# Optimization experiments

Measured on AMD Instinct MI355X. Metric: run time of the kernel, lower is better.

## Reference

```python
import jax, jax.numpy as jnp
import numpy as np

D_MODEL = 1024
N_HEADS = 16
D_HEAD = D_MODEL // N_HEADS


def setup_inputs() -> dict:
    key = jax.random.key(0)
    ks = jax.random.split(key, 5)
    B, T = 2, 2048
    x = jax.random.normal(ks[0], (B, T, D_MODEL), dtype=jnp.float32)
    s = 1.0 / np.sqrt(D_MODEL)
    W_qkv = jax.random.normal(ks[1], (D_MODEL, 3 * D_MODEL), dtype=jnp.float32) * s
    b_qkv = jnp.zeros((3 * D_MODEL,), dtype=jnp.float32)
    W_proj = jax.random.normal(ks[2], (D_MODEL, D_MODEL), dtype=jnp.float32) * s
    b_proj = jnp.zeros((D_MODEL,), dtype=jnp.float32)
    return {"x": x, "W_qkv": W_qkv, "b_qkv": b_qkv, "W_proj": W_proj, "b_proj": b_proj}


def reference(x, W_qkv, b_qkv, W_proj, b_proj):
    B, T, C = x.shape
    qkv = x @ W_qkv + b_qkv                      # [B,T,3C]
    q, k, v = jnp.split(qkv, 3, axis=-1)
    # [B,T,C] -> [B,H,T,Dh]
    def to_heads(t):
        return t.reshape(B, T, N_HEADS, D_HEAD).transpose(0, 2, 1, 3)
    q, k, v = to_heads(q), to_heads(k), to_heads(v)
    scale = 1.0 / np.sqrt(D_HEAD).astype(np.float32)
    scores = jnp.einsum('bhqd,bhkd->bhqk', q, k) * scale  # [B,H,T,T]
    causal = jnp.tril(jnp.ones((T, T), dtype=bool))
    scores = jnp.where(causal, scores, -jnp.inf)
    attn = jax.nn.softmax(scores, axis=-1)
    out = jnp.einsum('bhqk,bhkd->bhqd', attn, v)          # [B,H,T,Dh]
    out = out.transpose(0, 2, 1, 3).reshape(B, T, C)
    return out @ W_proj + b_proj
```

## Files before the change

kernel.cpp:

```cpp
#include <hip/hip_runtime.h>
#include <hip/hip_bf16.h>
#include <cstdint>


using u16 = unsigned short;
using u32 = unsigned int;

typedef __bf16 bf16x8 __attribute__((ext_vector_type(8)));
typedef float f32x4 __attribute__((ext_vector_type(4)));

#define AS1 __attribute__((address_space(1)))
#define AS3 __attribute__((address_space(3)))

__device__ __forceinline__ u16 f2bf(float f) {
  u32 u = __float_as_uint(f);
  u += 0x7fffu + ((u >> 16) & 1u);
  return (u16)(u >> 16);
}
__device__ __forceinline__ u32 cvtpk(float a, float b) {
  u32 r;
  asm("v_cvt_pk_bf16_f32 %0, %1, %2" : "=v"(r) : "v"(a), "v"(b));
  return r;
}

__global__ __launch_bounds__(256) void prep(const float* __restrict__ x,
                                            u16* __restrict__ xb,
                                            const float* __restrict__ W0,
                                            u16* __restrict__ T0,
                                            const float* __restrict__ W1,
                                            u16* __restrict__ T1) {
  const int bx = blockIdx.x;
  const int tid = threadIdx.x;
  if (bx < 4096) {
    const int i = bx * 256 + tid;
    float4 v = ((const float4*)x)[i];
    ushort4 o;
    o.x = f2bf(v.x); o.y = f2bf(v.y); o.z = f2bf(v.z); o.w = f2bf(v.w);
    ((ushort4*)xb)[i] = o;
    return;
  }
  __shared__ float t[32][33];
  const int idx = bx - 4096;
  const int bxx = idx & 127, by = idx >> 7;
  const float* W; u16* Wt; int N, n0;
  if (bxx < 96) { W = W0; Wt = T0; N = 3072; n0 = bxx * 32; }
  else          { W = W1; Wt = T1; N = 1024; n0 = (bxx - 96) * 32; }
  const int k0 = by * 32;
  const int tx = tid & 31, ty = tid >> 5;
#pragma unroll
  for (int i = 0; i < 4; ++i)
    t[ty + i * 8][tx] = W[(size_t)(k0 + ty + i * 8) * N + n0 + tx];
  __syncthreads();
#pragma unroll
  for (int i = 0; i < 4; ++i)
    Wt[(size_t)(n0 + ty + i * 8) * 1024 + k0 + tx] = f2bf(t[tx][ty + i * 8]);
}

#define MFMA16 __builtin_amdgcn_mfma_f32_16x16x32_bf16

__global__ __launch_bounds__(256, 2) void gemm_qkv(const u16* __restrict__ A,
                                                   const u16* __restrict__ Bt,
                                                   const float* __restrict__ bias,
                                                   u16* __restrict__ qb,
                                                   u16* __restrict__ KF,
                                                   u16* __restrict__ VF,
                                                   float sc_val) {
  constexpr int NT = 16;
  constexpr int BUFO = 5 * 4096;
  __shared__ __align__(16) u16 sm[2 * BUFO];

  const int tid  = threadIdx.x;
  const int lane = tid & 63;
  const int w    = tid >> 6;
  const int quad = lane >> 4;
  const int l15  = lane & 15;

  const int bid = blockIdx.x;
  const int xcd = bid & 7, c = bid >> 3;
  const int mt = xcd * 4 + (c & 3);
  const int nt = c >> 2;
  const int bm = mt * 128, bn = nt * 192;

  const int wc = w * 48;

  const int srow = tid >> 3;
  const int scol = (((tid & 7) ^ ((tid >> 3) & 7)) << 3);

#define STAGEA(ch, ktile, bufo)                                                 \
  do {                                                                          \
    const u16* _s = A + (size_t)(bm + (ch) * 64 + srow) * 1024 +                \
                    ((ktile) << 6) + scol;                                      \
    u16* _d = sm + (bufo) + (ch) * 4096 + tid * 8;                              \
    __builtin_amdgcn_global_load_lds((AS1 const void*)_s, (AS3 void*)_d,        \
                                     16, 0, 0);                                 \
    __builtin_amdgcn_global_load_lds((AS1 const void*)(_s + (32 << 10)),        \
                                     (AS3 void*)(_d + 2048), 16, 0, 0);         \
  } while (0)
#define STAGEB(ch, ktile, bufo)                                                 \
  do {                                                                          \
    const u16* _s = Bt + (size_t)(bn + (ch) * 64 + srow) * 1024 +               \
                    ((ktile) << 6) + scol;                                      \
    u16* _d = sm + (bufo) + (2 + (ch)) * 4096 + tid * 8;                        \
    __builtin_amdgcn_global_load_lds((AS1 const void*)_s, (AS3 void*)_d,        \
                                     16, 0, 0);                                 \
    __builtin_amdgcn_global_load_lds((AS1 const void*)(_s + (32 << 10)),        \
                                     (AS3 void*)(_d + 2048), 16, 0, 0);         \
  } while (0)

  int abase_lo[4], abase_hi[4], bbase[3];
#pragma unroll
  for (int mi = 0; mi < 4; ++mi) {
    abase_lo[mi] = 0 * 4096 + (mi * 16 + l15) * 64;
    abase_hi[mi] = 1 * 4096 + (mi * 16 + l15) * 64;
  }
#pragma unroll
  for (int ni = 0; ni < 3; ++ni) {
    const int rb = wc + ni * 16 + l15;
    bbase[ni] = (2 + (rb >> 6)) * 4096 + (rb & 63) * 64;
  }
  const int sw0 = ((quad ^ (l15 & 7)) << 3);
  const int sw1 = sw0 ^ 32;

  STAGEA(0, 0, 0); STAGEA(1, 0, 0);
  STAGEB(0, 0, 0); STAGEB(1, 0, 0); STAGEB(2, 0, 0);
  STAGEA(0, 1, BUFO); STAGEA(1, 1, BUFO);
  asm volatile("s_waitcnt vmcnt(4)" ::: "memory");
  __builtin_amdgcn_s_barrier();

  f32x4 acc[8][3] = {};
  bf16x8 alo[4][2], ahi[4][2], b[3][2];

#pragma unroll 2
  for (int j = 0; j < NT; ++j) {
    const int bo  = (j & 1) * BUFO;
    const int nbo = bo ^ BUFO;
    const u16* smb = sm + bo;

#pragma unroll
    for (int mi = 0; mi < 4; ++mi) {
      alo[mi][0] = *(const bf16x8*)(smb + abase_lo[mi] + sw0);
      alo[mi][1] = *(const bf16x8*)(smb + abase_lo[mi] + sw1);
    }
#pragma unroll
    for (int ni = 0; ni < 2; ++ni) {
      b[ni][0] = *(const bf16x8*)(smb + bbase[ni] + sw0);
      b[ni][1] = *(const bf16x8*)(smb + bbase[ni] + sw1);
    }
#pragma unroll
    for (int mi = 0; mi < 4; ++mi) {
      ahi[mi][0] = *(const bf16x8*)(smb + abase_hi[mi] + sw0);
      ahi[mi][1] = *(const bf16x8*)(smb + abase_hi[mi] + sw1);
    }
    b[2][0] = *(const bf16x8*)(smb + bbase[2] + sw0);
    b[2][1] = *(const bf16x8*)(smb + bbase[2] + sw1);
    if (j + 1 < NT) { STAGEB(0, j + 1, nbo); STAGEB(1, j + 1, nbo); STAGEB(2, j + 1, nbo); }

    asm volatile("s_waitcnt lgkmcnt(10)" ::: "memory");
    __builtin_amdgcn_sched_barrier(0);
    __builtin_amdgcn_s_setprio(1);
#pragma unroll
    for (int mi = 0; mi < 4; ++mi)
#pragma unroll
      for (int ni = 0; ni < 2; ++ni) {
        acc[mi][ni] = MFMA16(alo[mi][0], b[ni][0], acc[mi][ni], 0, 0, 0);
        acc[mi][ni] = MFMA16(alo[mi][1], b[ni][1], acc[mi][ni], 0, 0, 0);
      }
    __builtin_amdgcn_s_setprio(0);
    asm volatile("s_waitcnt lgkmcnt(0)" ::: "memory");
    __builtin_amdgcn_sched_barrier(0);
    __builtin_amdgcn_s_barrier();
    if (j + 2 < NT) { STAGEA(0, j + 2, bo); STAGEA(1, j + 2, bo); }
    __builtin_amdgcn_s_setprio(1);
#pragma unroll
    for (int mi = 0; mi < 4; ++mi) {
      acc[mi][2] = MFMA16(alo[mi][0], b[2][0], acc[mi][2], 0, 0, 0);
      acc[mi][2] = MFMA16(alo[mi][1], b[2][1], acc[mi][2], 0, 0, 0);
      acc[4 + mi][0] = MFMA16(ahi[mi][0], b[0][0], acc[4 + mi][0], 0, 0, 0);
      acc[4 + mi][0] = MFMA16(ahi[mi][1], b[0][1], acc[4 + mi][0], 0, 0, 0);
    }
#pragma unroll
    for (int mi = 0; mi < 4; ++mi)
#pragma unroll
      for (int ni = 1; ni < 3; ++ni) {
        acc[4 + mi][ni] = MFMA16(ahi[mi][0], b[ni][0], acc[4 + mi][ni], 0, 0, 0);
        acc[4 + mi][ni] = MFMA16(ahi[mi][1], b[ni][1], acc[4 + mi][ni], 0, 0, 0);
      }
    __builtin_amdgcn_s_setprio(0);
    if (j + 2 < NT)
      asm volatile("s_waitcnt vmcnt(4)" ::: "memory");
    else
      asm volatile("s_waitcnt vmcnt(0)" ::: "memory");
    __builtin_amdgcn_s_barrier();
  }
#undef STAGEA
#undef STAGEB

  const int crow0 = bm + (quad << 2);
  const int ccol0 = bn + wc + l15;
#pragma unroll
  for (int ni = 0; ni < 3; ++ni) {
    const int n = ccol0 + ni * 16;
    const float bv = bias[n];
    if (n < 1024) {
#pragma unroll
      for (int mi = 0; mi < 8; ++mi) {
        const int m0 = crow0 + mi * 16;
#pragma unroll
        for (int r = 0; r < 4; ++r)
          qb[(size_t)(m0 + r) * 1024 + n] = f2bf((acc[mi][ni][r] + bv) * sc_val);
      }
    } else if (n < 2048) {
      const int hk = (n - 1024) >> 6;
      const int d  = (n - 1024) & 63;
      const int hh = d >> 5, qd = (d >> 3) & 3, jj = d & 7;
#pragma unroll
      for (int mi = 0; mi < 8; ++mi) {
#pragma unroll
        for (int r = 0; r < 4; ++r) {
          const int t  = crow0 + mi * 16 + r;
          const int bb = t >> 11, tt = t & 2047;
          const int kt = tt >> 6, mm = (tt >> 4) & 3, l = tt & 15;
          KF[((size_t)((bb * 16 + hk) * 32 + kt) * 8 + mm * 2 + hh) * 512 +
             (qd * 16 + l) * 8 + jj] = f2bf(acc[mi][ni][r] + bv);
        }
      }
    } else {
      const int hv = (n - 2048) >> 6;
      const int d  = (n - 2048) & 63;
      const int di = d >> 4, l = d & 15;
#pragma unroll
      for (int mi = 0; mi < 8; ++mi) {
        const int t  = crow0 + mi * 16;
        const int bb = t >> 11, tt = t & 2047;
        const int kt = tt >> 6, to = tt & 63;
        const int mq = to >> 4, qd2 = (to >> 2) & 3;
        const int hh = mq >> 1, jj = (mq & 1) * 4;
        uint2 o;
        o.x = cvtpk(acc[mi][ni][0] + bv, acc[mi][ni][1] + bv);
        o.y = cvtpk(acc[mi][ni][2] + bv, acc[mi][ni][3] + bv);
        *(uint2*)&VF[((size_t)((bb * 16 + hv) * 32 + kt) * 8 + hh * 4 + di) * 512 +
                     (qd2 * 16 + l) * 8 + jj] = o;
      }
    }
  }
}

__global__ __launch_bounds__(256, 2) void gemm_proj(const u16* __restrict__ A,
                                                    const u16* __restrict__ Bt,
                                                    const float* __restrict__ bias,
                                                    float* __restrict__ C) {
  constexpr int NT = 16;
  constexpr int BUFO = 3 * 4096;
  __shared__ __align__(16) u16 sm[2 * BUFO];

  const int tid  = threadIdx.x;
  const int lane = tid & 63;
  const int w    = tid >> 6;
  const int quad = lane >> 4;
  const int l15  = lane & 15;

  const int bid = blockIdx.x;
  const int xcd = bid & 7, c = bid >> 3;
  const int mt = xcd * 4 + (c & 3);
  const int nt = c >> 2;
  const int bm = mt * 128, bn = nt * 64;

  const int wr = (w >> 1) * 64;
  const int wcC = (w & 1) * 32;

  const int srow = tid >> 3;
  const int scol = (((tid & 7) ^ ((tid >> 3) & 7)) << 3);

#define PSTAGEA(ch, ktile, bufo)                                                \
  do {                                                                          \
    const u16* _s = A + (size_t)(bm + (ch) * 64 + srow) * 1024 +                \
                    ((ktile) << 6) + scol;                                      \
    u16* _d = sm + (bufo) + (ch) * 4096 + tid * 8;                              \
    __builtin_amdgcn_global_load_lds((AS1 const void*)_s, (AS3 void*)_d,        \
                                     16, 0, 0);                                 \
    __builtin_amdgcn_global_load_lds((AS1 const void*)(_s + (32 << 10)),        \
                                     (AS3 void*)(_d + 2048), 16, 0, 0);         \
  } while (0)
#define PSTAGEB(ktile, bufo)                                                    \
  do {                                                                          \
    const u16* _s = Bt + (size_t)(bn + srow) * 1024 + ((ktile) << 6) + scol;    \
    u16* _d = sm + (bufo) + 2 * 4096 + tid * 8;                                 \
    __builtin_amdgcn_global_load_lds((AS1 const void*)_s, (AS3 void*)_d,        \
                                     16, 0, 0);                                 \
    __builtin_amdgcn_global_load_lds((AS1 const void*)(_s + (32 << 10)),        \
                                     (AS3 void*)(_d + 2048), 16, 0, 0);         \
  } while (0)

  int abase[4], bbase[2];
#pragma unroll
  for (int mi = 0; mi < 4; ++mi)
    abase[mi] = (w >> 1) * 4096 + (mi * 16 + l15) * 64;
#pragma unroll
  for (int ni = 0; ni < 2; ++ni)
    bbase[ni] = 2 * 4096 + (wcC + ni * 16 + l15) * 64;
  const int sw0 = ((quad ^ (l15 & 7)) << 3);
  const int sw1 = sw0 ^ 32;

  PSTAGEA(0, 0, 0); PSTAGEA(1, 0, 0); PSTAGEB(0, 0);
  PSTAGEA(0, 1, BUFO); PSTAGEA(1, 1, BUFO);
  asm volatile("s_waitcnt vmcnt(4)" ::: "memory");
  __builtin_amdgcn_s_barrier();

  f32x4 acc[4][2] = {};
  bf16x8 a[4][2], b[2][2];

#pragma unroll 2
  for (int j = 0; j < NT; ++j) {
    const int bo  = (j & 1) * BUFO;
    const int nbo = bo ^ BUFO;
    const u16* smb = sm + bo;

#pragma unroll
    for (int mi = 0; mi < 4; ++mi) {
      a[mi][0] = *(const bf16x8*)(smb + abase[mi] + sw0);
      a[mi][1] = *(const bf16x8*)(smb + abase[mi] + sw1);
    }
#pragma unroll
    for (int ni = 0; ni < 2; ++ni) {
      b[ni][0] = *(const bf16x8*)(smb + bbase[ni] + sw0);
      b[ni][1] = *(const bf16x8*)(smb + bbase[ni] + sw1);
    }
    if (j + 1 < NT) PSTAGEB(j + 1, nbo);

    asm volatile("s_waitcnt lgkmcnt(2)" ::: "memory");
    __builtin_amdgcn_sched_barrier(0);
    __builtin_amdgcn_s_setprio(1);
#pragma unroll
    for (int mi = 0; mi < 4; ++mi) {
      acc[mi][0] = MFMA16(a[mi][0], b[0][0], acc[mi][0], 0, 0, 0);
      acc[mi][0] = MFMA16(a[mi][1], b[0][1], acc[mi][0], 0, 0, 0);
    }
    __builtin_amdgcn_s_setprio(0);
    asm volatile("s_waitcnt lgkmcnt(0)" ::: "memory");
    __builtin_amdgcn_sched_barrier(0);
    __builtin_amdgcn_s_barrier();
    if (j + 2 < NT) { PSTAGEA(0, j + 2, bo); PSTAGEA(1, j + 2, bo); }
    __builtin_amdgcn_s_setprio(1);
#pragma unroll
    for (int mi = 0; mi < 4; ++mi) {
      acc[mi][1] = MFMA16(a[mi][0], b[1][0], acc[mi][1], 0, 0, 0);
      acc[mi][1] = MFMA16(a[mi][1], b[1][1], acc[mi][1], 0, 0, 0);
    }
    __builtin_amdgcn_s_setprio(0);
    if (j + 2 < NT)
      asm volatile("s_waitcnt vmcnt(4)" ::: "memory");
    else
      asm volatile("s_waitcnt vmcnt(0)" ::: "memory");
    __builtin_amdgcn_s_barrier();
  }
#undef PSTAGEA
#undef PSTAGEB

  const int crow0 = bm + wr + (quad << 2);
  const int ccol0 = bn + wcC + l15;
#pragma unroll
  for (int ni = 0; ni < 2; ++ni) {
    const int n = ccol0 + ni * 16;
    const float bv = bias[n];
#pragma unroll
    for (int mi = 0; mi < 4; ++mi) {
      const int m0 = crow0 + mi * 16;
#pragma unroll
      for (int r = 0; r < 4; ++r)
        C[(size_t)(m0 + r) * 1024 + n] = acc[mi][ni][r] + bv;
    }
  }
}

__global__ __launch_bounds__(128, 2) void attn_bal(const u16* __restrict__ qb,
                                                   const u16* __restrict__ KF,
                                                   const u16* __restrict__ VF,
                                                   u16* __restrict__ out) {
  const int bid = blockIdx.x;
  const int c   = bid >> 3;
  const int u   = c & 31;
  const int bh  = (bid & 7) | ((c >> 5) << 3);
  const int b = bh >> 4, h = bh & 15;
  const int tid = threadIdx.x;
  const int lane = tid & 63;
  const int par  = tid >> 6;
  const int quad = lane >> 4;
  const int l15  = lane & 15;

  __shared__ float CB[64][41];

  const u16* qbase = qb + (size_t)b * 2048 * 1024 + h * 64;
  const size_t fb = (size_t)bh * 32 * 4096 + lane * 8;
  const u16* kfb = KF + fb;
  const u16* vfb = VF + fb;

  union { u32 u4[4]; bf16x8 v; } onesu;
  onesu.u4[0] = onesu.u4[1] = onesu.u4[2] = onesu.u4[3] = 0x3f803f80u;
  const bf16x8 onesf = onesu.v;

  u16* const outb = out + (size_t)b * 2048 * 1024 + h * 64 + l15;

  auto run_group = [&](int g32) {
    const int q0 = g32 * 32;
    const int ktmax = g32 >> 1;

    bf16x8 qf[2][2];
#pragma unroll
    for (int g = 0; g < 2; ++g)
#pragma unroll
      for (int hh = 0; hh < 2; ++hh)
        qf[g][hh] = *(const bf16x8*)(qbase + (size_t)(q0 + g * 16 + l15) * 1024 +
                                     hh * 32 + quad * 8);

    f32x4 accO[2][4] = {};
    f32x4 accL[2] = {};

    bf16x8 kA[4][2], kB[4][2], vA[2][4], vB[2][4];
    {
      const u16* kp = kfb + (size_t)par * 4096;
      const u16* vp = vfb + (size_t)par * 4096;
#pragma unroll
      for (int m = 0; m < 4; ++m)
#pragma unroll
        for (int hh = 0; hh < 2; ++hh)
          kA[m][hh] = *(const bf16x8*)(kp + (m * 2 + hh) * 512);
#pragma unroll
      for (int hh = 0; hh < 2; ++hh)
#pragma unroll
        for (int di = 0; di < 4; ++di)
          vA[hh][di] = *(const bf16x8*)(vp + (hh * 4 + di) * 512);
    }

    auto tile = [&](int kt, bf16x8 (&KC)[4][2], bf16x8 (&KN)[4][2],
                    bf16x8 (&VC)[2][4], bf16x8 (&VN)[2][4]) {
      const int ktn = (kt + 2 <= ktmax) ? kt + 2 : ktmax;
      const u16* kpn = kfb + (size_t)ktn * 4096;
      const u16* vpn = vfb + (size_t)ktn * 4096;
#pragma unroll
      for (int m = 0; m < 4; ++m)
#pragma unroll
        for (int hh = 0; hh < 2; ++hh)
          KN[m][hh] = *(const bf16x8*)(kpn + (m * 2 + hh) * 512);
#pragma unroll
      for (int hh = 0; hh < 2; ++hh)
#pragma unroll
        for (int di = 0; di < 4; ++di)
          VN[hh][di] = *(const bf16x8*)(vpn + (hh * 4 + di) * 512);

      const bool diag = (kt == ktmax);
      bf16x8 ap[2][2];
#pragma unroll
      for (int g = 0; g < 2; ++g) {
        f32x4 sT[4] = {};
#pragma unroll
        for (int m = 0; m < 4; ++m) {
          sT[m] = MFMA16(KC[m][0], qf[g][0], sT[m], 0, 0, 0);
          sT[m] = MFMA16(KC[m][1], qf[g][1], sT[m], 0, 0, 0);
        }
        float pv[4][4];
        if (diag) {
          const int qgl = q0 + g * 16 + l15;
#pragma unroll
          for (int m = 0; m < 4; ++m)
#pragma unroll
            for (int r = 0; r < 4; ++r) {
              const bool msk = (kt * 64 + m * 16 + quad * 4 + r) > qgl;
              pv[m][r] = msk ? 0.f : __builtin_amdgcn_exp2f(sT[m][r]);
            }
        } else {
#pragma unroll
          for (int m = 0; m < 4; ++m)
#pragma unroll
            for (int r = 0; r < 4; ++r)
              pv[m][r] = __builtin_amdgcn_exp2f(sT[m][r]);
        }
        union { u32 u4[4]; bf16x8 v; } t0, t1;
        t0.u4[0] = cvtpk(pv[0][0], pv[0][1]);
        t0.u4[1] = cvtpk(pv[0][2], pv[0][3]);
        t0.u4[2] = cvtpk(pv[1][0], pv[1][1]);
        t0.u4[3] = cvtpk(pv[1][2], pv[1][3]);
        t1.u4[0] = cvtpk(pv[2][0], pv[2][1]);
        t1.u4[1] = cvtpk(pv[2][2], pv[2][3]);
        t1.u4[2] = cvtpk(pv[3][0], pv[3][1]);
        t1.u4[3] = cvtpk(pv[3][2], pv[3][3]);
        ap[g][0] = t0.v;
        ap[g][1] = t1.v;
      }

#pragma unroll
      for (int hh = 0; hh < 2; ++hh)
#pragma unroll
        for (int di = 0; di < 4; ++di) {
          bf16x8 bv = VC[hh][di];
#pragma unroll
          for (int g = 0; g < 2; ++g)
            accO[g][di] = MFMA16(ap[g][hh], bv, accO[g][di], 0, 0, 0);
        }
#pragma unroll
      for (int g = 0; g < 2; ++g) {
        accL[g] = MFMA16(ap[g][0], onesf, accL[g], 0, 0, 0);
        accL[g] = MFMA16(ap[g][1], onesf, accL[g], 0, 0, 0);
      }
    };

    for (int kt = par; kt <= ktmax; ) {
      tile(kt, kA, kB, vA, vB); kt += 2;
      if (kt > ktmax) break;
      tile(kt, kB, kA, vB, vA); kt += 2;
    }

    if (par) {
      float* cb = CB[lane];
#pragma unroll
      for (int g = 0; g < 2; ++g) {
#pragma unroll
        for (int di = 0; di < 4; ++di)
#pragma unroll
          for (int r = 0; r < 4; ++r)
            cb[g * 16 + di * 4 + r] = accO[g][di][r];
#pragma unroll
        for (int r = 0; r < 4; ++r)
          cb[32 + g * 4 + r] = accL[g][r];
      }
    }
    __syncthreads();
    if (!par) {
      const float* cb = CB[lane];
#pragma unroll
      for (int g = 0; g < 2; ++g) {
#pragma unroll
        for (int di = 0; di < 4; ++di)
#pragma unroll
          for (int r = 0; r < 4; ++r)
            accO[g][di][r] += cb[g * 16 + di * 4 + r];
#pragma unroll
        for (int r = 0; r < 4; ++r)
          accL[g][r] += cb[32 + g * 4 + r];
      }
#pragma unroll
      for (int g = 0; g < 2; ++g)
#pragma unroll
        for (int r = 0; r < 4; ++r) {
          const float inv = 1.f / accL[g][r];
          const int q = q0 + g * 16 + quad * 4 + r;
          u16* op = outb + (size_t)q * 1024;
#pragma unroll
          for (int di = 0; di < 4; ++di)
            op[di * 16] = f2bf(accO[g][di][r] * inv);
        }
    }
    __syncthreads();
  };

  run_group(63 - u);
  run_group(u);
}

extern "C" void kernel_launch(void* const* d_in, const int* in_sizes, int n_in,
                              void* d_out, int out_size, void* d_ws, size_t ws_size,
                              hipStream_t stream) {
  const float* x     = (const float*)d_in[0];
  const float* Wqkv  = (const float*)d_in[1];
  const float* bqkv  = (const float*)d_in[2];
  const float* Wproj = (const float*)d_in[3];
  const float* bproj = (const float*)d_in[4];
  float* out = (float*)d_out;

  char* ws = (char*)d_ws;
  u16* xb     = (u16*)(ws);
  u16* wqkvT  = (u16*)(ws + 8388608);
  u16* wprojT = (u16*)(ws + 14680064);
  u16* qb     = (u16*)(ws + 16777216);
  u16* KF     = (u16*)(ws + 25165824);
  u16* VF     = (u16*)(ws + 33554432);
  u16* att    = (u16*)(ws + 41943040);

  constexpr float cs = 0.18033688011f;

  prep<<<8192, 256, 0, stream>>>(x, xb, Wqkv, wqkvT, Wproj, wprojT);

  gemm_qkv<<<dim3(512), 256, 0, stream>>>(xb, wqkvT, bqkv, qb, KF, VF, cs);

  attn_bal<<<dim3(1024), 128, 0, stream>>>(qb, KF, VF, att);

  gemm_proj<<<dim3(512), 256, 0, stream>>>(att, wprojT, bproj, out);
}
```

Measured before the change: 152.3 us.

## Split QKV GEMM tile across eight waves instead of four

Moves the QKV projection GEMM from 256 to 512 threads per block. Each wave now computes a 64x48 sub-tile instead of 128x48, and each thread issues one async global-to-LDS load per chunk instead of two. Accumulator and fragment register use per wave is halved to allow more waves per CU and better latency hiding. In exchange, each wave does less MFMA work per LDS read and barrier, and more threads take part in each block-wide sync.

```diff
diff --git a/kernel.cpp b/kernel.cpp
--- a/kernel.cpp
+++ b/kernel.cpp
@@ -58,7 +58,7 @@
 
 #define MFMA16 __builtin_amdgcn_mfma_f32_16x16x32_bf16
 
-__global__ __launch_bounds__(256, 2) void gemm_qkv(const u16* __restrict__ A,
+__global__ __launch_bounds__(512, 4) void gemm_qkv(const u16* __restrict__ A,
                                                    const u16* __restrict__ Bt,
                                                    const float* __restrict__ bias,
                                                    u16* __restrict__ qb,
@@ -81,41 +81,30 @@
   const int nt = c >> 2;
   const int bm = mt * 128, bn = nt * 192;
 
-  const int wc = w * 48;
+  const int wr  = (w >> 2) * 64;
+  const int wc2 = (w & 3) * 48;
 
   const int srow = tid >> 3;
   const int scol = (((tid & 7) ^ ((tid >> 3) & 7)) << 3);
 
 #define STAGEA(ch, ktile, bufo)                                                 \
-  do {                                                                          \
-    const u16* _s = A + (size_t)(bm + (ch) * 64 + srow) * 1024 +                \
-                    ((ktile) << 6) + scol;                                      \
-    u16* _d = sm + (bufo) + (ch) * 4096 + tid * 8;                              \
-    __builtin_amdgcn_global_load_lds((AS1 const void*)_s, (AS3 void*)_d,        \
-                                     16, 0, 0);                                 \
-    __builtin_amdgcn_global_load_lds((AS1 const void*)(_s + (32 << 10)),        \
-                                     (AS3 void*)(_d + 2048), 16, 0, 0);         \
-  } while (0)
+  __builtin_amdgcn_global_load_lds(                                             \
+      (AS1 const void*)(A + (size_t)(bm + (ch) * 64 + srow) * 1024 +            \
+                        ((ktile) << 6) + scol),                                 \
+      (AS3 void*)(sm + (bufo) + (ch) * 4096 + tid * 8), 16, 0, 0)
 #define STAGEB(ch, ktile, bufo)                                                 \
-  do {                                                                          \
-    const u16* _s = Bt + (size_t)(bn + (ch) * 64 + srow) * 1024 +               \
-                    ((ktile) << 6) + scol;                                      \
-    u16* _d = sm + (bufo) + (2 + (ch)) * 4096 + tid * 8;                        \
-    __builtin_amdgcn_global_load_lds((AS1 const void*)_s, (AS3 void*)_d,        \
-                                     16, 0, 0);                                 \
-    __builtin_amdgcn_global_load_lds((AS1 const void*)(_s + (32 << 10)),        \
-                                     (AS3 void*)(_d + 2048), 16, 0, 0);         \
-  } while (0)
-
-  int abase_lo[4], abase_hi[4], bbase[3];
-#pragma unroll
-  for (int mi = 0; mi < 4; ++mi) {
-    abase_lo[mi] = 0 * 4096 + (mi * 16 + l15) * 64;
-    abase_hi[mi] = 1 * 4096 + (mi * 16 + l15) * 64;
-  }
+  __builtin_amdgcn_global_load_lds(                                             \
+      (AS1 const void*)(Bt + (size_t)(bn + (ch) * 64 + srow) * 1024 +           \
+                        ((ktile) << 6) + scol),                                 \
+      (AS3 void*)(sm + (bufo) + (2 + (ch)) * 4096 + tid * 8), 16, 0, 0)
+
+  int abase[4], bbase[3];
+#pragma unroll
+  for (int mi = 0; mi < 4; ++mi)
+    abase[mi] = (w >> 2) * 4096 + (mi * 16 + l15) * 64;
 #pragma unroll
   for (int ni = 0; ni < 3; ++ni) {
-    const int rb = wc + ni * 16 + l15;
+    const int rb = wc2 + ni * 16 + l15;
     bbase[ni] = (2 + (rb >> 6)) * 4096 + (rb & 63) * 64;
   }
   const int sw0 = ((quad ^ (l15 & 7)) << 3);
@@ -124,11 +113,11 @@
   STAGEA(0, 0, 0); STAGEA(1, 0, 0);
   STAGEB(0, 0, 0); STAGEB(1, 0, 0); STAGEB(2, 0, 0);
   STAGEA(0, 1, BUFO); STAGEA(1, 1, BUFO);
-  asm volatile("s_waitcnt vmcnt(4)" ::: "memory");
+  asm volatile("s_waitcnt vmcnt(2)" ::: "memory");
   __builtin_amdgcn_s_barrier();
 
-  f32x4 acc[8][3] = {};
-  bf16x8 alo[4][2], ahi[4][2], b[3][2];
+  f32x4 acc[4][3] = {};
+  bf16x8 a[4][2], b[3][2];
 
 #pragma unroll 2
   for (int j = 0; j < NT; ++j) {
@@ -138,33 +127,24 @@
 
 #pragma unroll
     for (int mi = 0; mi < 4; ++mi) {
-      alo[mi][0] = *(const bf16x8*)(smb + abase_lo[mi] + sw0);
-      alo[mi][1] = *(const bf16x8*)(smb + abase_lo[mi] + sw1);
-    }
-#pragma unroll
-    for (int ni = 0; ni < 2; ++ni) {
+      a[mi][0] = *(const bf16x8*)(smb + abase[mi] + sw0);
+      a[mi][1] = *(const bf16x8*)(smb + abase[mi] + sw1);
+    }
+#pragma unroll
+    for (int ni = 0; ni < 3; ++ni) {
       b[ni][0] = *(const bf16x8*)(smb + bbase[ni] + sw0);
       b[ni][1] = *(const bf16x8*)(smb + bbase[ni] + sw1);
     }
-#pragma unroll
-    for (int mi = 0; mi < 4; ++mi) {
-      ahi[mi][0] = *(const bf16x8*)(smb + abase_hi[mi] + sw0);
-      ahi[mi][1] = *(const bf16x8*)(smb + abase_hi[mi] + sw1);
-    }
-    b[2][0] = *(const bf16x8*)(smb + bbase[2] + sw0);
-    b[2][1] = *(const bf16x8*)(smb + bbase[2] + sw1);
     if (j + 1 < NT) { STAGEB(0, j + 1, nbo); STAGEB(1, j + 1, nbo); STAGEB(2, j + 1, nbo); }
 
-    asm volatile("s_waitcnt lgkmcnt(10)" ::: "memory");
+    asm volatile("s_waitcnt lgkmcnt(4)" ::: "memory");
     __builtin_amdgcn_sched_barrier(0);
     __builtin_amdgcn_s_setprio(1);
 #pragma unroll
-    for (int mi = 0; mi < 4; ++mi)
-#pragma unroll
-      for (int ni = 0; ni < 2; ++ni) {
-        acc[mi][ni] = MFMA16(alo[mi][0], b[ni][0], acc[mi][ni], 0, 0, 0);
-        acc[mi][ni] = MFMA16(alo[mi][1], b[ni][1], acc[mi][ni], 0, 0, 0);
-      }
+    for (int mi = 0; mi < 4; ++mi) {
+      acc[mi][0] = MFMA16(a[mi][0], b[0][0], acc[mi][0], 0, 0, 0);
+      acc[mi][0] = MFMA16(a[mi][1], b[0][1], acc[mi][0], 0, 0, 0);
+    }
     __builtin_amdgcn_s_setprio(0);
     asm volatile("s_waitcnt lgkmcnt(0)" ::: "memory");
     __builtin_amdgcn_sched_barrier(0);
@@ -173,21 +153,14 @@
     __builtin_amdgcn_s_setprio(1);
 #pragma unroll
     for (int mi = 0; mi < 4; ++mi) {
-      acc[mi][2] = MFMA16(alo[mi][0], b[2][0], acc[mi][2], 0, 0, 0);
-      acc[mi][2] = MFMA16(alo[mi][1], b[2][1], acc[mi][2], 0, 0, 0);
-      acc[4 + mi][0] = MFMA16(ahi[mi][0], b[0][0], acc[4 + mi][0], 0, 0, 0);
-      acc[4 + mi][0] = MFMA16(ahi[mi][1], b[0][1], acc[4 + mi][0], 0, 0, 0);
-    }
-#pragma unroll
-    for (int mi = 0; mi < 4; ++mi)
-#pragma unroll
-      for (int ni = 1; ni < 3; ++ni) {
-        acc[4 + mi][ni] = MFMA16(ahi[mi][0], b[ni][0], acc[4 + mi][ni], 0, 0, 0);
-        acc[4 + mi][ni] = MFMA16(ahi[mi][1], b[ni][1], acc[4 + mi][ni], 0, 0, 0);
-      }
+      acc[mi][1] = MFMA16(a[mi][0], b[1][0], acc[mi][1], 0, 0, 0);
+      acc[mi][1] = MFMA16(a[mi][1], b[1][1], acc[mi][1], 0, 0, 0);
+      acc[mi][2] = MFMA16(a[mi][0], b[2][0], acc[mi][2], 0, 0, 0);
+      acc[mi][2] = MFMA16(a[mi][1], b[2][1], acc[mi][2], 0, 0, 0);
+    }
     __builtin_amdgcn_s_setprio(0);
     if (j + 2 < NT)
-      asm volatile("s_waitcnt vmcnt(4)" ::: "memory");
+      asm volatile("s_waitcnt vmcnt(2)" ::: "memory");
     else
       asm volatile("s_waitcnt vmcnt(0)" ::: "memory");
     __builtin_amdgcn_s_barrier();
@@ -195,15 +168,15 @@
 #undef STAGEA
 #undef STAGEB
 
-  const int crow0 = bm + (quad << 2);
-  const int ccol0 = bn + wc + l15;
+  const int crow0 = bm + wr + (quad << 2);
+  const int ccol0 = bn + wc2 + l15;
 #pragma unroll
   for (int ni = 0; ni < 3; ++ni) {
     const int n = ccol0 + ni * 16;
     const float bv = bias[n];
     if (n < 1024) {
 #pragma unroll
-      for (int mi = 0; mi < 8; ++mi) {
+      for (int mi = 0; mi < 4; ++mi) {
         const int m0 = crow0 + mi * 16;
 #pragma unroll
         for (int r = 0; r < 4; ++r)
@@ -214,7 +187,7 @@
       const int d  = (n - 1024) & 63;
       const int hh = d >> 5, qd = (d >> 3) & 3, jj = d & 7;
 #pragma unroll
-      for (int mi = 0; mi < 8; ++mi) {
+      for (int mi = 0; mi < 4; ++mi) {
 #pragma unroll
         for (int r = 0; r < 4; ++r) {
           const int t  = crow0 + mi * 16 + r;
@@ -229,7 +202,7 @@
       const int d  = (n - 2048) & 63;
       const int di = d >> 4, l = d & 15;
 #pragma unroll
-      for (int mi = 0; mi < 8; ++mi) {
+      for (int mi = 0; mi < 4; ++mi) {
         const int t  = crow0 + mi * 16;
         const int bb = t >> 11, tt = t & 2047;
         const int kt = tt >> 6, to = tt & 63;
@@ -579,7 +552,7 @@
 
   prep<<<8192, 256, 0, stream>>>(x, xb, Wqkv, wqkvT, Wproj, wprojT);
 
-  gemm_qkv<<<dim3(512), 256, 0, stream>>>(xb, wqkvT, bqkv, qb, KF, VF, cs);
+  gemm_qkv<<<dim3(512), 512, 0, stream>>>(xb, wqkvT, bqkv, qb, KF, VF, cs);
 
   attn_bal<<<dim3(1024), 128, 0, stream>>>(qb, KF, VF, att);
 
```

Measured after the change: 156.7 us. +2.8%, slower.
